# Kernel tuning notes

Measured on AMD Instinct MI355X. Metric: run time of the kernel, lower is better.

## Reference

```python
import jax, jax.numpy as jnp
import numpy as np

TOP_K = 2
SCALING = 32.0 / 16.0  # lora_alpha / r

N, D, O = 4096, 4096, 4096   # tokens, in_features, out_features
E, H, R_RANK = 8, 3, 16      # experts, B-heads per expert, lora rank
W_SCALE = 0.02               # keep logits in a sane range


def setup_inputs() -> dict:
    key = jax.random.key(0)
    ks = jax.random.split(key, 6)
    return {
        "x": jax.random.normal(ks[0], (N, D), jnp.float32),
        "base_W": jax.random.normal(ks[1], (D, O), jnp.float32) * W_SCALE,
        "router_W": jax.random.normal(ks[2], (E, D), jnp.float32) * W_SCALE,
        "A": jax.random.normal(ks[3], (E, D, R_RANK), jnp.float32) * W_SCALE,
        "B": jax.random.normal(ks[4], (E, H, R_RANK, O), jnp.float32) * W_SCALE,
        "R": jax.random.normal(ks[5], (E, D, H), jnp.float32) * W_SCALE,
    }


def reference(x, base_W, router_W, A, B, R):
    # Base dense layer
    base = x @ base_W                                   # [N, O]
    # Expert router: softmax over experts, top-k gate renormalized
    probs = jax.nn.softmax(x @ router_W.T, axis=-1)     # [N, E]
    topv, topi = jax.lax.top_k(probs, TOP_K)            # [N, k]
    topv = topv / topv.sum(-1, keepdims=True)
    n_idx = jnp.arange(x.shape[0])[:, None]
    gate = jnp.zeros_like(probs).at[n_idx, topi].set(topv)  # dense [N, E] gate, 0 off top-k
    # Shared lora_A per expert
    a = jnp.einsum('nd,edr->ner', x, A)                 # [N, E, r]
    # Per-expert head router over lora_B heads
    head_w = jax.nn.softmax(jnp.einsum('nd,edh->neh', x, R), axis=-1)  # [N, E, H]
    # Head-weighted B projections, combined with expert gates
    delta = jnp.einsum('ner,neh,ehro,ne->no', a, head_w, B, gate)      # [N, O]
    return base + SCALING * delta
```

## Files before the change

kernel.cpp:

```cpp
#include <hip/hip_runtime.h>
#include <hip/hip_bf16.h>
#include <math.h>

typedef __bf16 bf16_t;
typedef __bf16 bf16x4_t __attribute__((ext_vector_type(4)));
typedef __bf16 bf16x8_t __attribute__((ext_vector_type(8)));
typedef float  f32x4_t  __attribute__((ext_vector_type(4)));

#define N_TOK 4096
#define D_IN  4096
#define O_OUT 4096
#define NEXP  8
#define NHEAD 3
#define RANK  16
#define KC2   384
#define PCOLS 256
#define SCALING_F 2.0f


__device__ __forceinline__ void transpose_tile(const float* __restrict__ src,
                                               bf16_t* __restrict__ dst,
                                               int Rr, int Cc, int r0, int c0,
                                               float (*tile)[65]) {
  int q  = threadIdx.x & 15;
  int r4 = threadIdx.x >> 4;
  #pragma unroll
  for (int g = 0; g < 4; ++g) {
    int r = r4 + g * 16;
    float4 v = *(const float4*)(src + (size_t)(r0 + r) * Cc + c0 + q * 4);
    tile[r][q * 4 + 0] = v.x; tile[r][q * 4 + 1] = v.y;
    tile[r][q * 4 + 2] = v.z; tile[r][q * 4 + 3] = v.w;
  }
  __syncthreads();
  #pragma unroll
  for (int g = 0; g < 4; ++g) {
    int c = r4 + g * 16;
    bf16x4_t o = { (bf16_t)tile[q * 4 + 0][c], (bf16_t)tile[q * 4 + 1][c],
                   (bf16_t)tile[q * 4 + 2][c], (bf16_t)tile[q * 4 + 3][c] };
    *(bf16x4_t*)(dst + (size_t)(c0 + c) * Rr + r0 + q * 4) = o;
  }
}

__global__ __launch_bounds__(256) void prep_kernel(const float* __restrict__ x,
                                                   const float* __restrict__ base_W,
                                                   const float* __restrict__ rw,
                                                   const float* __restrict__ A,
                                                   const float* __restrict__ B,
                                                   const float* __restrict__ Rm,
                                                   bf16_t* __restrict__ xb,
                                                   bf16_t* __restrict__ WbT,
                                                   bf16_t* __restrict__ BbT,
                                                   bf16_t* __restrict__ PabT,
                                                   int* __restrict__ gidx,
                                                   float* __restrict__ gwv) {
  __shared__ float tile[64][65];
  int b = blockIdx.x;
  if (b < 4096) {
    transpose_tile(base_W, WbT, 4096, 4096, (b & 63) * 64, (b >> 6) * 64, tile);
  } else if (b < 5120) {
    int lane = threadIdx.x & 63;
    int wv = threadIdx.x >> 6;
    int n = (b - 4096) * 4 + wv;
    const float4* xv = (const float4*)(x + (size_t)n * D_IN);
    bf16x4_t* xo = (bf16x4_t*)(xb + (size_t)n * D_IN);
    float acc[NEXP] = {0, 0, 0, 0, 0, 0, 0, 0};
    for (int d = lane; d < D_IN / 4; d += 64) {
      float4 xx = xv[d];
      bf16x4_t ob = { (bf16_t)xx.x, (bf16_t)xx.y, (bf16_t)xx.z, (bf16_t)xx.w };
      xo[d] = ob;
      #pragma unroll
      for (int e = 0; e < NEXP; ++e) {
        float4 ww = ((const float4*)(rw + (size_t)e * D_IN))[d];
        acc[e] += xx.x * ww.x + xx.y * ww.y + xx.z * ww.z + xx.w * ww.w;
      }
    }
    #pragma unroll
    for (int e = 0; e < NEXP; ++e) {
      float v = acc[e];
      #pragma unroll
      for (int o = 32; o > 0; o >>= 1) v += __shfl_down(v, o);
      acc[e] = v;
    }
    if (lane == 0) {
      int i0 = 0; float l0 = acc[0];
      #pragma unroll
      for (int e = 1; e < NEXP; ++e) if (acc[e] > l0) { l0 = acc[e]; i0 = e; }
      int i1 = -1; float l1 = -3.4e38f;
      #pragma unroll
      for (int e = 0; e < NEXP; ++e) if (e != i0 && acc[e] > l1) { l1 = acc[e]; i1 = e; }
      float w0 = 1.f / (1.f + expf(l1 - l0));
      gidx[2 * n] = i0; gidx[2 * n + 1] = i1;
      gwv[2 * n] = w0;  gwv[2 * n + 1] = 1.f - w0;
    }
  } else if (b < 5504) {
    int t = b - 5120;
    transpose_tile(B, BbT, KC2, 4096, (t % 6) * 64, (t / 6) * 64, tile);
  } else {
    int c = b - 5504;
    for (int d = threadIdx.x; d < D_IN; d += 256) {
      float v = 0.f;
      if (c < 128) {
        int e = c >> 4, r = c & 15;
        v = A[((size_t)e * D_IN + d) * RANK + r];
      } else if (c < 152) {
        int qq = c - 128; int e = qq / 3, h = qq - 3 * e;
        v = Rm[((size_t)e * D_IN + d) * NHEAD + h];
      }
      PabT[(size_t)c * D_IN + d] = (bf16_t)v;
    }
  }
}

__global__ void gating_kernel(const float* __restrict__ projP, const int* __restrict__ gidx,
                              const float* __restrict__ gwv, bf16_t* __restrict__ C2b) {
  int n = blockIdx.x;
  int c = threadIdx.x;
  int e = c / 48;
  int h = (c % 48) / 16;
  int r = c & 15;
  int i0 = gidx[2 * n], i1 = gidx[2 * n + 1];
  float g = (e == i0) ? gwv[2 * n] : (e == i1) ? gwv[2 * n + 1] : 0.f;
  float val = 0.f;
  if (g != 0.f) {
    const float* p0 = projP + (size_t)n * PCOLS;
    const size_t S = (size_t)N_TOK * PCOLS;
    #define RD(cc) (p0[(cc)] + p0[(cc) + S] + p0[(cc) + 2 * S] + p0[(cc) + 3 * S])
    float h0 = RD(128 + e * 3 + 0);
    float h1 = RD(128 + e * 3 + 1);
    float h2 = RD(128 + e * 3 + 2);
    float av = RD(e * 16 + r);
    #undef RD
    float mx = fmaxf(h0, fmaxf(h1, h2));
    float e0 = expf(h0 - mx), e1 = expf(h1 - mx), e2 = expf(h2 - mx);
    float hw = (h == 0 ? e0 : h == 1 ? e1 : e2) / (e0 + e1 + e2);
    val = SCALING_F * g * hw * av;
  }
  C2b[(size_t)n * KC2 + c] = (bf16_t)val;
}

__device__ __forceinline__ void run_kloop(f32x4_t (&acc)[4][4], bf16_t* sA, bf16_t* sB,
                                          const bf16_t* __restrict__ Ab, int lda,
                                          const bf16_t* __restrict__ Bb, int ldb, int K) {
  const int tid = threadIdx.x;
  const int lane = tid & 63;
  const int w = tid >> 6;
  const int wm = (w >> 1) * 64;
  const int wn = (w & 1) * 64;
  const int qd = lane >> 4;
  const int ln = lane & 15;
  const int sw = ln & 7;

  size_t offA[4], offB[4];
  int lo[4];
  #pragma unroll
  for (int t = 0; t < 4; ++t) {
    int c = tid + t * 256;
    int m = c >> 3, kc = (c & 7) ^ (m & 7);
    offA[t] = (size_t)m * lda + kc * 8;
    offB[t] = (size_t)m * ldb + kc * 8;
    lo[t] = c * 8;
  }
  int rowA[4], rowB[4];
  #pragma unroll
  for (int i = 0; i < 4; ++i) {
    rowA[i] = (wm + i * 16 + ln) * 64;
    rowB[i] = (wn + i * 16 + ln) * 64;
  }

  for (int k0 = 0; k0 < K; k0 += 64) {
    __syncthreads();
    #pragma unroll
    for (int t = 0; t < 4; ++t)
      __builtin_amdgcn_global_load_lds(
          (const __attribute__((address_space(1))) void*)(Ab + k0 + offA[t]),
          (__attribute__((address_space(3))) void*)(sA + lo[t]), 16, 0, 0);
    #pragma unroll
    for (int t = 0; t < 4; ++t)
      __builtin_amdgcn_global_load_lds(
          (const __attribute__((address_space(1))) void*)(Bb + k0 + offB[t]),
          (__attribute__((address_space(3))) void*)(sB + lo[t]), 16, 0, 0);
    __syncthreads();
    #pragma unroll
    for (int s = 0; s < 2; ++s) {
      bf16x8_t af[4], bfr[4];
      int kx = ((s * 4 + qd) ^ sw) * 8;
      #pragma unroll
      for (int i = 0; i < 4; ++i) af[i]  = *(const bf16x8_t*)(sA + rowA[i] + kx);
      #pragma unroll
      for (int i = 0; i < 4; ++i) bfr[i] = *(const bf16x8_t*)(sB + rowB[i] + kx);
      #pragma unroll
      for (int i = 0; i < 4; ++i)
        #pragma unroll
        for (int j = 0; j < 4; ++j)
          acc[i][j] = __builtin_amdgcn_mfma_f32_16x16x32_bf16(af[i], bfr[j], acc[i][j], 0, 0, 0);
    }
  }
}

__global__ __launch_bounds__(256) void gemm_proj_kernel(const bf16_t* __restrict__ xb,
                                                        const bf16_t* __restrict__ PabT,
                                                        float* __restrict__ projP) {
  __shared__ bf16_t sA[128 * 64];
  __shared__ bf16_t sB[128 * 64];
  int bm = blockIdx.x, bn = blockIdx.y, kz = blockIdx.z;
  f32x4_t acc[4][4] = {};
  run_kloop(acc, sA, sB,
            xb + (size_t)bm * 128 * D_IN + kz * 1024, D_IN,
            PabT + (size_t)bn * 128 * D_IN + kz * 1024, D_IN, 1024);
  const int lane = threadIdx.x & 63, w = threadIdx.x >> 6;
  const int wm = (w >> 1) * 64, wn = (w & 1) * 64, qd = lane >> 4, ln = lane & 15;
  float* Cb = projP + (size_t)kz * N_TOK * PCOLS + (size_t)bm * 128 * PCOLS + bn * 128;
  #pragma unroll
  for (int i = 0; i < 4; ++i)
    #pragma unroll
    for (int j = 0; j < 4; ++j) {
      int col = wn + j * 16 + ln;
      #pragma unroll
      for (int rg = 0; rg < 4; ++rg) {
        int row = wm + i * 16 + qd * 4 + rg;
        Cb[(size_t)row * PCOLS + col] = acc[i][j][rg];
      }
    }
}

__global__ __launch_bounds__(256) void gemm_fused_kernel(const bf16_t* __restrict__ xb,
                                                         const bf16_t* __restrict__ WbT,
                                                         const bf16_t* __restrict__ C2b,
                                                         const bf16_t* __restrict__ BbT,
                                                         float* __restrict__ out) {
  __shared__ bf16_t sA[128 * 64];
  __shared__ bf16_t sB[128 * 64];
  int bm = blockIdx.x, bn = blockIdx.y;
  f32x4_t acc[4][4] = {};
  run_kloop(acc, sA, sB,
            xb + (size_t)bm * 128 * D_IN, D_IN,
            WbT + (size_t)bn * 128 * D_IN, D_IN, D_IN);
  run_kloop(acc, sA, sB,
            C2b + (size_t)bm * 128 * KC2, KC2,
            BbT + (size_t)bn * 128 * KC2, KC2, KC2);
  const int lane = threadIdx.x & 63, w = threadIdx.x >> 6;
  const int wm = (w >> 1) * 64, wn = (w & 1) * 64, qd = lane >> 4, ln = lane & 15;
  float* Cb = out + (size_t)bm * 128 * O_OUT + bn * 128;
  #pragma unroll
  for (int i = 0; i < 4; ++i)
    #pragma unroll
    for (int j = 0; j < 4; ++j) {
      int col = wn + j * 16 + ln;
      #pragma unroll
      for (int rg = 0; rg < 4; ++rg) {
        int row = wm + i * 16 + qd * 4 + rg;
        Cb[(size_t)row * O_OUT + col] = acc[i][j][rg];
      }
    }
}

extern "C" void kernel_launch(void* const* d_in, const int* in_sizes, int n_in,
                              void* d_out, int out_size, void* d_ws, size_t ws_size,
                              hipStream_t stream) {
  const float* x       = (const float*)d_in[0];
  const float* base_W  = (const float*)d_in[1];
  const float* routerW = (const float*)d_in[2];
  const float* A       = (const float*)d_in[3];
  const float* B       = (const float*)d_in[4];
  const float* Rm      = (const float*)d_in[5];
  float* out = (float*)d_out;
  char* ws = (char*)d_ws;

  bf16_t* xb   = (bf16_t*)(ws);
  bf16_t* WbT  = (bf16_t*)(ws + 33554432);
  bf16_t* PabT = (bf16_t*)(ws + 67108864);
  bf16_t* BbT  = (bf16_t*)(ws + 69206016);
  bf16_t* C2b  = (bf16_t*)(ws + 72351744);
  int*    gidx = (int*)   (ws + 75497472);
  float*  gwv  = (float*) (ws + 75530240);
  float*  projP = out;

  prep_kernel<<<5760, 256, 0, stream>>>(x, base_W, routerW, A, B, Rm,
                                        xb, WbT, BbT, PabT, gidx, gwv);
  gemm_proj_kernel<<<dim3(32, 2, 4), 256, 0, stream>>>(xb, PabT, projP);
  gating_kernel<<<4096, 384, 0, stream>>>(projP, gidx, gwv, C2b);
  gemm_fused_kernel<<<dim3(32, 32), 256, 0, stream>>>(xb, WbT, C2b, BbT, out);
}
```

Measured before the change: 414.9 us.

## Merge all stages into one persistent kernel with software grid barriers

```diff
diff --git a/kernel.cpp b/kernel.cpp
--- a/kernel.cpp
+++ b/kernel.cpp
@@ -16,7 +16,24 @@
 #define KC2   384
 #define PCOLS 256
 #define SCALING_F 2.0f
-
+#define NBLK  512
+#define SPLITK 8
+
+__device__ __forceinline__ void grid_barrier(unsigned* cnt, unsigned* gen) {
+  __syncthreads();
+  if (threadIdx.x == 0) {
+    __threadfence();
+    unsigned old = __hip_atomic_fetch_add(cnt, 1u, __ATOMIC_ACQ_REL, __HIP_MEMORY_SCOPE_AGENT);
+    if (old == NBLK - 1) {
+      __hip_atomic_store(gen, 1u, __ATOMIC_RELEASE, __HIP_MEMORY_SCOPE_AGENT);
+    } else {
+      while (!__hip_atomic_load(gen, __ATOMIC_ACQUIRE, __HIP_MEMORY_SCOPE_AGENT))
+        __builtin_amdgcn_s_sleep(8);
+    }
+    __threadfence();
+  }
+  __syncthreads();
+}
 
 __device__ __forceinline__ void transpose_tile(const float* __restrict__ src,
                                                bf16_t* __restrict__ dst,
@@ -39,103 +56,7 @@
                    (bf16_t)tile[q * 4 + 2][c], (bf16_t)tile[q * 4 + 3][c] };
     *(bf16x4_t*)(dst + (size_t)(c0 + c) * Rr + r0 + q * 4) = o;
   }
-}
-
-__global__ __launch_bounds__(256) void prep_kernel(const float* __restrict__ x,
-                                                   const float* __restrict__ base_W,
-                                                   const float* __restrict__ rw,
-                                                   const float* __restrict__ A,
-                                                   const float* __restrict__ B,
-                                                   const float* __restrict__ Rm,
-                                                   bf16_t* __restrict__ xb,
-                                                   bf16_t* __restrict__ WbT,
-                                                   bf16_t* __restrict__ BbT,
-                                                   bf16_t* __restrict__ PabT,
-                                                   int* __restrict__ gidx,
-                                                   float* __restrict__ gwv) {
-  __shared__ float tile[64][65];
-  int b = blockIdx.x;
-  if (b < 4096) {
-    transpose_tile(base_W, WbT, 4096, 4096, (b & 63) * 64, (b >> 6) * 64, tile);
-  } else if (b < 5120) {
-    int lane = threadIdx.x & 63;
-    int wv = threadIdx.x >> 6;
-    int n = (b - 4096) * 4 + wv;
-    const float4* xv = (const float4*)(x + (size_t)n * D_IN);
-    bf16x4_t* xo = (bf16x4_t*)(xb + (size_t)n * D_IN);
-    float acc[NEXP] = {0, 0, 0, 0, 0, 0, 0, 0};
-    for (int d = lane; d < D_IN / 4; d += 64) {
-      float4 xx = xv[d];
-      bf16x4_t ob = { (bf16_t)xx.x, (bf16_t)xx.y, (bf16_t)xx.z, (bf16_t)xx.w };
-      xo[d] = ob;
-      #pragma unroll
-      for (int e = 0; e < NEXP; ++e) {
-        float4 ww = ((const float4*)(rw + (size_t)e * D_IN))[d];
-        acc[e] += xx.x * ww.x + xx.y * ww.y + xx.z * ww.z + xx.w * ww.w;
-      }
-    }
-    #pragma unroll
-    for (int e = 0; e < NEXP; ++e) {
-      float v = acc[e];
-      #pragma unroll
-      for (int o = 32; o > 0; o >>= 1) v += __shfl_down(v, o);
-      acc[e] = v;
-    }
-    if (lane == 0) {
-      int i0 = 0; float l0 = acc[0];
-      #pragma unroll
-      for (int e = 1; e < NEXP; ++e) if (acc[e] > l0) { l0 = acc[e]; i0 = e; }
-      int i1 = -1; float l1 = -3.4e38f;
-      #pragma unroll
-      for (int e = 0; e < NEXP; ++e) if (e != i0 && acc[e] > l1) { l1 = acc[e]; i1 = e; }
-      float w0 = 1.f / (1.f + expf(l1 - l0));
-      gidx[2 * n] = i0; gidx[2 * n + 1] = i1;
-      gwv[2 * n] = w0;  gwv[2 * n + 1] = 1.f - w0;
-    }
-  } else if (b < 5504) {
-    int t = b - 5120;
-    transpose_tile(B, BbT, KC2, 4096, (t % 6) * 64, (t / 6) * 64, tile);
-  } else {
-    int c = b - 5504;
-    for (int d = threadIdx.x; d < D_IN; d += 256) {
-      float v = 0.f;
-      if (c < 128) {
-        int e = c >> 4, r = c & 15;
-        v = A[((size_t)e * D_IN + d) * RANK + r];
-      } else if (c < 152) {
-        int qq = c - 128; int e = qq / 3, h = qq - 3 * e;
-        v = Rm[((size_t)e * D_IN + d) * NHEAD + h];
-      }
-      PabT[(size_t)c * D_IN + d] = (bf16_t)v;
-    }
-  }
-}
-
-__global__ void gating_kernel(const float* __restrict__ projP, const int* __restrict__ gidx,
-                              const float* __restrict__ gwv, bf16_t* __restrict__ C2b) {
-  int n = blockIdx.x;
-  int c = threadIdx.x;
-  int e = c / 48;
-  int h = (c % 48) / 16;
-  int r = c & 15;
-  int i0 = gidx[2 * n], i1 = gidx[2 * n + 1];
-  float g = (e == i0) ? gwv[2 * n] : (e == i1) ? gwv[2 * n + 1] : 0.f;
-  float val = 0.f;
-  if (g != 0.f) {
-    const float* p0 = projP + (size_t)n * PCOLS;
-    const size_t S = (size_t)N_TOK * PCOLS;
-    #define RD(cc) (p0[(cc)] + p0[(cc) + S] + p0[(cc) + 2 * S] + p0[(cc) + 3 * S])
-    float h0 = RD(128 + e * 3 + 0);
-    float h1 = RD(128 + e * 3 + 1);
-    float h2 = RD(128 + e * 3 + 2);
-    float av = RD(e * 16 + r);
-    #undef RD
-    float mx = fmaxf(h0, fmaxf(h1, h2));
-    float e0 = expf(h0 - mx), e1 = expf(h1 - mx), e2 = expf(h2 - mx);
-    float hw = (h == 0 ? e0 : h == 1 ? e1 : e2) / (e0 + e1 + e2);
-    val = SCALING_F * g * hw * av;
-  }
-  C2b[(size_t)n * KC2 + c] = (bf16_t)val;
+  __syncthreads();
 }
 
 __device__ __forceinline__ void run_kloop(f32x4_t (&acc)[4][4], bf16_t* sA, bf16_t* sB,
@@ -197,61 +118,177 @@
   }
 }
 
-__global__ __launch_bounds__(256) void gemm_proj_kernel(const bf16_t* __restrict__ xb,
-                                                        const bf16_t* __restrict__ PabT,
-                                                        float* __restrict__ projP) {
-  __shared__ bf16_t sA[128 * 64];
-  __shared__ bf16_t sB[128 * 64];
-  int bm = blockIdx.x, bn = blockIdx.y, kz = blockIdx.z;
-  f32x4_t acc[4][4] = {};
-  run_kloop(acc, sA, sB,
-            xb + (size_t)bm * 128 * D_IN + kz * 1024, D_IN,
-            PabT + (size_t)bn * 128 * D_IN + kz * 1024, D_IN, 1024);
-  const int lane = threadIdx.x & 63, w = threadIdx.x >> 6;
-  const int wm = (w >> 1) * 64, wn = (w & 1) * 64, qd = lane >> 4, ln = lane & 15;
-  float* Cb = projP + (size_t)kz * N_TOK * PCOLS + (size_t)bm * 128 * PCOLS + bn * 128;
-  #pragma unroll
-  for (int i = 0; i < 4; ++i)
-    #pragma unroll
-    for (int j = 0; j < 4; ++j) {
-      int col = wn + j * 16 + ln;
-      #pragma unroll
-      for (int rg = 0; rg < 4; ++rg) {
-        int row = wm + i * 16 + qd * 4 + rg;
-        Cb[(size_t)row * PCOLS + col] = acc[i][j][rg];
-      }
-    }
-}
-
-__global__ __launch_bounds__(256) void gemm_fused_kernel(const bf16_t* __restrict__ xb,
-                                                         const bf16_t* __restrict__ WbT,
-                                                         const bf16_t* __restrict__ C2b,
-                                                         const bf16_t* __restrict__ BbT,
-                                                         float* __restrict__ out) {
-  __shared__ bf16_t sA[128 * 64];
-  __shared__ bf16_t sB[128 * 64];
-  int bm = blockIdx.x, bn = blockIdx.y;
-  f32x4_t acc[4][4] = {};
-  run_kloop(acc, sA, sB,
-            xb + (size_t)bm * 128 * D_IN, D_IN,
-            WbT + (size_t)bn * 128 * D_IN, D_IN, D_IN);
-  run_kloop(acc, sA, sB,
-            C2b + (size_t)bm * 128 * KC2, KC2,
-            BbT + (size_t)bn * 128 * KC2, KC2, KC2);
-  const int lane = threadIdx.x & 63, w = threadIdx.x >> 6;
-  const int wm = (w >> 1) * 64, wn = (w & 1) * 64, qd = lane >> 4, ln = lane & 15;
-  float* Cb = out + (size_t)bm * 128 * O_OUT + bn * 128;
-  #pragma unroll
-  for (int i = 0; i < 4; ++i)
-    #pragma unroll
-    for (int j = 0; j < 4; ++j) {
-      int col = wn + j * 16 + ln;
-      #pragma unroll
-      for (int rg = 0; rg < 4; ++rg) {
-        int row = wm + i * 16 + qd * 4 + rg;
-        Cb[(size_t)row * O_OUT + col] = acc[i][j][rg];
-      }
-    }
+__global__ __launch_bounds__(256) void mono_kernel(const float* __restrict__ x,
+                                                   const float* __restrict__ base_W,
+                                                   const float* __restrict__ rw,
+                                                   const float* __restrict__ A,
+                                                   const float* __restrict__ B,
+                                                   const float* __restrict__ Rm,
+                                                   bf16_t* __restrict__ xb,
+                                                   bf16_t* __restrict__ WbT,
+                                                   bf16_t* __restrict__ BbT,
+                                                   bf16_t* __restrict__ PabT,
+                                                   bf16_t* __restrict__ C2b,
+                                                   int* __restrict__ gidx,
+                                                   float* __restrict__ gwv,
+                                                   float* __restrict__ projP,
+                                                   float* __restrict__ out,
+                                                   unsigned* __restrict__ bar) {
+  __shared__ __align__(16) char smem[32768];
+  float (*tile)[65] = (float(*)[65])smem;
+  bf16_t* sA = (bf16_t*)smem;
+  bf16_t* sB = (bf16_t*)(smem + 16384);
+  const int blk = blockIdx.x;
+  const int tid = threadIdx.x;
+
+  #pragma unroll
+  for (int i = 0; i < 8; ++i) {
+    int t = blk * 8 + i;
+    transpose_tile(base_W, WbT, 4096, 4096, (t & 63) * 64, (t >> 6) * 64, tile);
+  }
+  if (blk < 384) transpose_tile(B, BbT, KC2, 4096, (blk % 6) * 64, (blk / 6) * 64, tile);
+  if (blk < 256) {
+    int c = blk;
+    for (int d = tid; d < D_IN; d += 256) {
+      float v = 0.f;
+      if (c < 128) {
+        int e = c >> 4, r = c & 15;
+        v = A[((size_t)e * D_IN + d) * RANK + r];
+      } else if (c < 152) {
+        int qq = c - 128; int e = qq / 3, h = qq - 3 * e;
+        v = Rm[((size_t)e * D_IN + d) * NHEAD + h];
+      }
+      PabT[(size_t)c * D_IN + d] = (bf16_t)v;
+    }
+  }
+  {
+    int lane = tid & 63;
+    int wv = tid >> 6;
+    #pragma unroll
+    for (int it = 0; it < 2; ++it) {
+      int n = blk * 8 + it * 4 + wv;
+      const float4* xv = (const float4*)(x + (size_t)n * D_IN);
+      bf16x4_t* xo = (bf16x4_t*)(xb + (size_t)n * D_IN);
+      float acc[NEXP] = {0, 0, 0, 0, 0, 0, 0, 0};
+      for (int d = lane; d < D_IN / 4; d += 64) {
+        float4 xx = xv[d];
+        bf16x4_t ob = { (bf16_t)xx.x, (bf16_t)xx.y, (bf16_t)xx.z, (bf16_t)xx.w };
+        xo[d] = ob;
+        #pragma unroll
+        for (int e = 0; e < NEXP; ++e) {
+          float4 ww = ((const float4*)(rw + (size_t)e * D_IN))[d];
+          acc[e] += xx.x * ww.x + xx.y * ww.y + xx.z * ww.z + xx.w * ww.w;
+        }
+      }
+      #pragma unroll
+      for (int e = 0; e < NEXP; ++e) {
+        float v = acc[e];
+        #pragma unroll
+        for (int o = 32; o > 0; o >>= 1) v += __shfl_down(v, o);
+        acc[e] = v;
+      }
+      if (lane == 0) {
+        int i0 = 0; float l0 = acc[0];
+        #pragma unroll
+        for (int e = 1; e < NEXP; ++e) if (acc[e] > l0) { l0 = acc[e]; i0 = e; }
+        int i1 = -1; float l1 = -3.4e38f;
+        #pragma unroll
+        for (int e = 0; e < NEXP; ++e) if (e != i0 && acc[e] > l1) { l1 = acc[e]; i1 = e; }
+        float w0 = 1.f / (1.f + expf(l1 - l0));
+        gidx[2 * n] = i0; gidx[2 * n + 1] = i1;
+        gwv[2 * n] = w0;  gwv[2 * n + 1] = 1.f - w0;
+      }
+    }
+  }
+
+  grid_barrier(bar + 0, bar + 1);
+
+  {
+    int kz = blk >> 6;
+    int rem = blk & 63;
+    int bm = rem >> 1, bn = rem & 1;
+    f32x4_t acc[4][4] = {};
+    run_kloop(acc, sA, sB,
+              xb + (size_t)bm * 128 * D_IN + kz * 512, D_IN,
+              PabT + (size_t)bn * 128 * D_IN + kz * 512, D_IN, 512);
+    const int lane = tid & 63, w = tid >> 6;
+    const int wm = (w >> 1) * 64, wn = (w & 1) * 64, qd = lane >> 4, ln = lane & 15;
+    float* Cb = projP + (size_t)kz * N_TOK * PCOLS + (size_t)bm * 128 * PCOLS + bn * 128;
+    #pragma unroll
+    for (int i = 0; i < 4; ++i)
+      #pragma unroll
+      for (int j = 0; j < 4; ++j) {
+        int col = wn + j * 16 + ln;
+        #pragma unroll
+        for (int rg = 0; rg < 4; ++rg)
+          Cb[(size_t)(wm + i * 16 + qd * 4 + rg) * PCOLS + col] = acc[i][j][rg];
+      }
+  }
+
+  grid_barrier(bar + 2, bar + 3);
+
+  {
+    const size_t S = (size_t)N_TOK * PCOLS;
+    for (int tt = 0; tt < 8; ++tt) {
+      int n = blk * 8 + tt;
+      int i0 = gidx[2 * n], i1 = gidx[2 * n + 1];
+      float g0 = gwv[2 * n], g1 = gwv[2 * n + 1];
+      const float* p0 = projP + (size_t)n * PCOLS;
+      for (int c = tid; c < KC2; c += 256) {
+        int e = c / 48;
+        int h = (c % 48) / 16;
+        int r = c & 15;
+        float g = (e == i0) ? g0 : (e == i1) ? g1 : 0.f;
+        float val = 0.f;
+        if (g != 0.f) {
+          float h0 = 0.f, h1 = 0.f, h2 = 0.f, av = 0.f;
+          #pragma unroll
+          for (int p = 0; p < SPLITK; ++p) {
+            const float* pp = p0 + p * S;
+            h0 += pp[128 + e * 3 + 0];
+            h1 += pp[128 + e * 3 + 1];
+            h2 += pp[128 + e * 3 + 2];
+            av += pp[e * 16 + r];
+          }
+          float mx = fmaxf(h0, fmaxf(h1, h2));
+          float e0 = expf(h0 - mx), e1 = expf(h1 - mx), e2 = expf(h2 - mx);
+          float hw = (h == 0 ? e0 : h == 1 ? e1 : e2) / (e0 + e1 + e2);
+          val = SCALING_F * g * hw * av;
+        }
+        C2b[(size_t)n * KC2 + c] = (bf16_t)val;
+      }
+    }
+  }
+
+  grid_barrier(bar + 4, bar + 5);
+
+  {
+    int bm = blk & 31;
+    int bnp = (blk >> 5) * 2;
+    for (int t = 0; t < 2; ++t) {
+      int bn = bnp + t;
+      f32x4_t acc[4][4] = {};
+      run_kloop(acc, sA, sB,
+                xb + (size_t)bm * 128 * D_IN, D_IN,
+                WbT + (size_t)bn * 128 * D_IN, D_IN, D_IN);
+      run_kloop(acc, sA, sB,
+                C2b + (size_t)bm * 128 * KC2, KC2,
+                BbT + (size_t)bn * 128 * KC2, KC2, KC2);
+      const int lane = tid & 63, w = tid >> 6;
+      const int wm = (w >> 1) * 64, wn = (w & 1) * 64, qd = lane >> 4, ln = lane & 15;
+      float* Cb = out + (size_t)bm * 128 * O_OUT + bn * 128;
+      #pragma unroll
+      for (int i = 0; i < 4; ++i)
+        #pragma unroll
+        for (int j = 0; j < 4; ++j) {
+          int col = wn + j * 16 + ln;
+          #pragma unroll
+          for (int rg = 0; rg < 4; ++rg)
+            Cb[(size_t)(wm + i * 16 + qd * 4 + rg) * O_OUT + col] = acc[i][j][rg];
+        }
+      __syncthreads();
+    }
+  }
 }
 
 extern "C" void kernel_launch(void* const* d_in, const int* in_sizes, int n_in,
@@ -273,11 +310,11 @@
   bf16_t* C2b  = (bf16_t*)(ws + 72351744);
   int*    gidx = (int*)   (ws + 75497472);
   float*  gwv  = (float*) (ws + 75530240);
-  float*  projP = out;
-
-  prep_kernel<<<5760, 256, 0, stream>>>(x, base_W, routerW, A, B, Rm,
-                                        xb, WbT, BbT, PabT, gidx, gwv);
-  gemm_proj_kernel<<<dim3(32, 2, 4), 256, 0, stream>>>(xb, PabT, projP);
-  gating_kernel<<<4096, 384, 0, stream>>>(projP, gidx, gwv, C2b);
-  gemm_fused_kernel<<<dim3(32, 32), 256, 0, stream>>>(xb, WbT, C2b, BbT, out);
-}
+  unsigned* bar = (unsigned*)(ws + 75563008);
+  float* projP = out;
+
+  hipMemsetAsync(bar, 0, 64, stream);
+  mono_kernel<<<NBLK, 256, 0, stream>>>(x, base_W, routerW, A, B, Rm,
+                                        xb, WbT, BbT, PabT, C2b, gidx, gwv,
+                                        projP, out, bar);
+}
```

Result: slower. 676.6 us (+63.1%).
